# Performance work log

Measured on AMD Instinct MI355X. Metric: run time of the kernel, lower is better.

## Reference

```python
import jax, jax.numpy as jnp
import numpy as np

B, L, F = 16, 2048, 512


def setup_inputs() -> dict:
    key = jax.random.key(0)
    k1, k2 = jax.random.split(key)
    feature = jax.random.normal(k1, (B, L, F), dtype=jnp.float32)
    noise = jax.random.normal(k2, (B, L, L), dtype=jnp.float32)
    return {"feature": feature, "noise": noise}


def reference(feature, noise):
    # augmenting_path = softmax over last dim of (B, L, L) gaussian noise
    augmenting_path = jax.nn.softmax(noise, axis=-1)
    # einsum 'bij,bjf->bif': mix frames along the sequence dim
    augmented_feature = jnp.einsum('bij,bjf->bif', augmenting_path, feature)
    return augmented_feature
```

## Files before the change

kernel.cpp:

```cpp
#include <hip/hip_runtime.h>
#include <hip/hip_bf16.h>


#define NB 16
#define SL 2048
#define NF 512
#define TM 64
#define BK 32
#define NT 512

typedef __bf16 bf16x8 __attribute__((ext_vector_type(8)));
typedef float  f32x4  __attribute__((ext_vector_type(4)));

__device__ __forceinline__ unsigned short f2bf(float x) {
    union { float f; unsigned int u; } v; v.f = x;
    return (unsigned short)((v.u + 0x7FFFu + ((v.u >> 16) & 1u)) >> 16);
}

__global__ __launch_bounds__(256, 4)
void feat_panelize(const float* __restrict__ feat, unsigned short* __restrict__ featP) {
    __shared__ unsigned short Lt[32][270];
    const int t  = threadIdx.x;
    const int n0 = blockIdx.x * 256;
    const int kb = blockIdx.y;
    const int b  = blockIdx.z;
    const float* src = feat + ((size_t)b * SL + (size_t)kb * BK) * NF + n0;
    const int j  = t >> 3;
    const int c0 = (t & 7) << 2;
    #pragma unroll
    for (int c = 0; c < 8; ++c) {
        const float4 v = *(const float4*)(src + (size_t)j * NF + c0 + (c << 5));
        unsigned short* p = &Lt[j][c0 + (c << 5)];
        p[0] = f2bf(v.x); p[1] = f2bf(v.y); p[2] = f2bf(v.z); p[3] = f2bf(v.w);
    }
    __syncthreads();
    unsigned int w[16];
    #pragma unroll
    for (int m = 0; m < 16; ++m)
        w[m] = (unsigned int)Lt[2 * m][t] | ((unsigned int)Lt[2 * m + 1][t] << 16);
    unsigned short* dst = featP + ((size_t)(b * 64 + kb) * NF + (size_t)(n0 + t)) * BK;
    #pragma unroll
    for (int c = 0; c < 4; ++c)
        *(uint4*)(dst + (c << 3)) = *(const uint4*)&w[c << 2];
}

__global__ __launch_bounds__(NT, 2)
void frame_augment(const float* __restrict__ noise,
                   const unsigned short* __restrict__ featP,
                   float* __restrict__ out) {
    __shared__ __align__(16) unsigned short As[TM][40];
    __shared__ __align__(16) unsigned short Bs[NF][40];
    __shared__ float part[TM][9];
    __shared__ float linv[TM];

    const int tid  = threadIdx.x;
    const int lane = tid & 63;
    const int wv   = tid >> 6;
    const int b    = blockIdx.y;
    const int i0   = blockIdx.x * TM;

    const float* noise_b = noise + ((size_t)b * SL + i0) * SL;
    float*       out_b   = out   + ((size_t)b * SL + i0) * NF;

    const int a_row = tid >> 3;
    const int a_col = (tid & 7) << 2;
    const int fm = lane & 15;
    const int fq = lane >> 4;

    f32x4 acc[4][4];
    #pragma unroll
    for (int mi = 0; mi < 4; ++mi)
        #pragma unroll
        for (int ni = 0; ni < 4; ++ni)
            acc[mi][ni] = (f32x4){0.f, 0.f, 0.f, 0.f};

    float rowsum = 0.f;
    const float* a_src = noise_b + (size_t)a_row * SL + a_col;

    for (int kb = 0; kb < SL / BK; ++kb) {
        const float4 nv = *(const float4*)(a_src + kb * BK);
        const float e0 = __expf(nv.x), e1 = __expf(nv.y);
        const float e2 = __expf(nv.z), e3 = __expf(nv.w);
        rowsum += (e0 + e1) + (e2 + e3);
        uint2 ap;
        ap.x = (unsigned int)f2bf(e0) | ((unsigned int)f2bf(e1) << 16);
        ap.y = (unsigned int)f2bf(e2) | ((unsigned int)f2bf(e3) << 16);
        *(uint2*)&As[a_row][a_col] = ap;

        const unsigned short* panel = featP + (size_t)(b * 64 + kb) * NF * BK;
        #pragma unroll
        for (int c = 0; c < 4; ++c) {
            const int q = tid + (c << 9);
            const uint4 d = *(const uint4*)(panel + (size_t)q * 8);
            *(uint4*)&Bs[q >> 2][(q & 3) << 3] = d;
        }
        __syncthreads();

        bf16x8 af[4], bfr[4];
        #pragma unroll
        for (int mi = 0; mi < 4; ++mi)
            af[mi] = *(const bf16x8*)&As[mi * 16 + fm][fq << 3];
        #pragma unroll
        for (int ni = 0; ni < 4; ++ni)
            bfr[ni] = *(const bf16x8*)&Bs[(wv << 6) + ni * 16 + fm][fq << 3];
        #pragma unroll
        for (int mi = 0; mi < 4; ++mi)
            #pragma unroll
            for (int ni = 0; ni < 4; ++ni)
                acc[mi][ni] = __builtin_amdgcn_mfma_f32_16x16x32_bf16(
                    af[mi], bfr[ni], acc[mi][ni], 0, 0, 0);
        __syncthreads();
    }

    part[a_row][tid & 7] = rowsum;
    __syncthreads();
    if (tid < TM) {
        float s = 0.f;
        #pragma unroll
        for (int q = 0; q < 8; ++q) s += part[tid][q];
        linv[tid] = 1.0f / s;
    }
    __syncthreads();

    #pragma unroll
    for (int mi = 0; mi < 4; ++mi) {
        #pragma unroll
        for (int r = 0; r < 4; ++r) {
            const int row = mi * 16 + (fq << 2) + r;
            const float sc = linv[row];
            float* orow = out_b + (size_t)row * NF + (wv << 6) + fm;
            #pragma unroll
            for (int ni = 0; ni < 4; ++ni)
                orow[ni * 16] = acc[mi][ni][r] * sc;
        }
    }
}

extern "C" void kernel_launch(void* const* d_in, const int* in_sizes, int n_in,
                              void* d_out, int out_size, void* d_ws, size_t ws_size,
                              hipStream_t stream) {
    (void)in_sizes; (void)n_in; (void)out_size; (void)ws_size;
    const float* feat  = (const float*)d_in[0];
    const float* noise = (const float*)d_in[1];
    float* outp = (float*)d_out;
    unsigned short* featP = (unsigned short*)d_ws;

    feat_panelize<<<dim3(NF / 256, SL / BK, NB), 256, 0, stream>>>(feat, featP);
    frame_augment<<<dim3(SL / TM, NB), NT, 0, stream>>>(noise, featP, outp);
}
```

Measured before the change: 469.0 us.

## Double-buffer LDS with direct global-to-LDS loads, double M tile, remap blocks

The main GEMM kernel now uses double-buffered LDS tiles. The feature panel for the next K step is loaded straight into LDS with global_load_lds, and the noise for two steps ahead is prefetched into registers, so loads overlap the MFMA work. The row tile grows from 64 to 128, which halves how often each block re-reads the feature panels, and the grid is flattened with a batch-interleaved block order to improve L2 locality. The LDS rows lose their padding, which may cause bank conflicts. The larger accumulator also raises register pressure and could reduce occupancy.

```diff
diff --git a/kernel.cpp b/kernel.cpp
--- a/kernel.cpp
+++ b/kernel.cpp
@@ -5,16 +5,17 @@
 #define NB 16
 #define SL 2048
 #define NF 512
-#define TM 64
+#define TM 128
 #define BK 32
 #define NT 512
+#define NKB (SL / BK)
 
 typedef __bf16 bf16x8 __attribute__((ext_vector_type(8)));
 typedef float  f32x4  __attribute__((ext_vector_type(4)));
 
-__device__ __forceinline__ unsigned short f2bf(float x) {
+__device__ __forceinline__ unsigned int f2bf(float x) {
     union { float f; unsigned int u; } v; v.f = x;
-    return (unsigned short)((v.u + 0x7FFFu + ((v.u >> 16) & 1u)) >> 16);
+    return (v.u + 0x7FFFu + ((v.u >> 16) & 1u)) >> 16;
 }
 
 __global__ __launch_bounds__(256, 4)
@@ -31,14 +32,15 @@
     for (int c = 0; c < 8; ++c) {
         const float4 v = *(const float4*)(src + (size_t)j * NF + c0 + (c << 5));
         unsigned short* p = &Lt[j][c0 + (c << 5)];
-        p[0] = f2bf(v.x); p[1] = f2bf(v.y); p[2] = f2bf(v.z); p[3] = f2bf(v.w);
+        p[0] = (unsigned short)f2bf(v.x); p[1] = (unsigned short)f2bf(v.y);
+        p[2] = (unsigned short)f2bf(v.z); p[3] = (unsigned short)f2bf(v.w);
     }
     __syncthreads();
     unsigned int w[16];
     #pragma unroll
     for (int m = 0; m < 16; ++m)
         w[m] = (unsigned int)Lt[2 * m][t] | ((unsigned int)Lt[2 * m + 1][t] << 16);
-    unsigned short* dst = featP + ((size_t)(b * 64 + kb) * NF + (size_t)(n0 + t)) * BK;
+    unsigned short* dst = featP + ((size_t)(b * NKB + kb) * NF + (size_t)(n0 + t)) * BK;
     #pragma unroll
     for (int c = 0; c < 4; ++c)
         *(uint4*)(dst + (c << 3)) = *(const uint4*)&w[c << 2];
@@ -48,63 +50,98 @@
 void frame_augment(const float* __restrict__ noise,
                    const unsigned short* __restrict__ featP,
                    float* __restrict__ out) {
-    __shared__ __align__(16) unsigned short As[TM][40];
-    __shared__ __align__(16) unsigned short Bs[NF][40];
-    __shared__ float part[TM][9];
+    __shared__ __align__(16) unsigned short As[2][TM][BK];
+    __shared__ __align__(16) unsigned short Bs[2][NF][BK];
+    __shared__ float part[TM][4];
     __shared__ float linv[TM];
 
     const int tid  = threadIdx.x;
     const int lane = tid & 63;
     const int wv   = tid >> 6;
-    const int b    = blockIdx.y;
-    const int i0   = blockIdx.x * TM;
+    const int n    = blockIdx.x;
+    const int b    = ((n & 7) << 1) | ((n >> 3) & 1);
+    const int i0   = (n >> 4) * TM;
 
     const float* noise_b = noise + ((size_t)b * SL + i0) * SL;
-    float*       out_b   = out   + ((size_t)b * SL + i0) * NF;
+    const unsigned short* featB = featP + (size_t)b * NKB * NF * BK;
+    float* out_b = out + ((size_t)b * SL + i0) * NF;
 
-    const int a_row = tid >> 3;
-    const int a_col = (tid & 7) << 2;
+    const int ar = tid >> 2;
+    const int ac = (tid & 3) << 3;
     const int fm = lane & 15;
     const int fq = lane >> 4;
 
-    f32x4 acc[4][4];
+    f32x4 acc[8][4];
     #pragma unroll
-    for (int mi = 0; mi < 4; ++mi)
+    for (int mi = 0; mi < 8; ++mi)
         #pragma unroll
         for (int ni = 0; ni < 4; ++ni)
             acc[mi][ni] = (f32x4){0.f, 0.f, 0.f, 0.f};
 
     float rowsum = 0.f;
-    const float* a_src = noise_b + (size_t)a_row * SL + a_col;
+    const float* a_src = noise_b + (size_t)ar * SL + ac;
 
-    for (int kb = 0; kb < SL / BK; ++kb) {
-        const float4 nv = *(const float4*)(a_src + kb * BK);
-        const float e0 = __expf(nv.x), e1 = __expf(nv.y);
-        const float e2 = __expf(nv.z), e3 = __expf(nv.w);
-        rowsum += (e0 + e1) + (e2 + e3);
-        uint2 ap;
-        ap.x = (unsigned int)f2bf(e0) | ((unsigned int)f2bf(e1) << 16);
-        ap.y = (unsigned int)f2bf(e2) | ((unsigned int)f2bf(e3) << 16);
-        *(uint2*)&As[a_row][a_col] = ap;
-
-        const unsigned short* panel = featP + (size_t)(b * 64 + kb) * NF * BK;
+    float4 nv0 = *(const float4*)(a_src);
+    float4 nv1 = *(const float4*)(a_src + 4);
+    {
+        const float e0=__expf(nv0.x), e1=__expf(nv0.y), e2=__expf(nv0.z), e3=__expf(nv0.w);
+        const float e4=__expf(nv1.x), e5=__expf(nv1.y), e6=__expf(nv1.z), e7=__expf(nv1.w);
+        rowsum += ((e0+e1)+(e2+e3)) + ((e4+e5)+(e6+e7));
+        uint4 p;
+        p.x = f2bf(e0) | (f2bf(e1) << 16);  p.y = f2bf(e2) | (f2bf(e3) << 16);
+        p.z = f2bf(e4) | (f2bf(e5) << 16);  p.w = f2bf(e6) | (f2bf(e7) << 16);
+        *(uint4*)&As[0][ar][ac] = p;
+    }
+    {
+        const unsigned short* panel = featB;
         #pragma unroll
         for (int c = 0; c < 4; ++c) {
-            const int q = tid + (c << 9);
-            const uint4 d = *(const uint4*)(panel + (size_t)q * 8);
-            *(uint4*)&Bs[q >> 2][(q & 3) << 3] = d;
+            const int q = (c << 9) + tid;
+            __builtin_amdgcn_global_load_lds(
+                (const __attribute__((address_space(1))) unsigned int*)(panel + (size_t)q * 8),
+                (__attribute__((address_space(3))) unsigned int*)&Bs[0][q >> 2][(q & 3) << 3],
+                16, 0, 0);
         }
-        __syncthreads();
+    }
+    nv0 = *(const float4*)(a_src + BK);
+    nv1 = *(const float4*)(a_src + BK + 4);
+    __syncthreads();
 
-        bf16x8 af[4], bfr[4];
+    for (int kb = 0; kb < NKB; ++kb) {
+        const int cur = kb & 1, nxt = cur ^ 1;
+
+        if (kb + 1 < NKB) {
+            const unsigned short* panel = featB + (size_t)(kb + 1) * NF * BK;
+            #pragma unroll
+            for (int c = 0; c < 4; ++c) {
+                const int q = (c << 9) + tid;
+                __builtin_amdgcn_global_load_lds(
+                    (const __attribute__((address_space(1))) unsigned int*)(panel + (size_t)q * 8),
+                    (__attribute__((address_space(3))) unsigned int*)&Bs[nxt][q >> 2][(q & 3) << 3],
+                    16, 0, 0);
+            }
+            const float e0=__expf(nv0.x), e1=__expf(nv0.y), e2=__expf(nv0.z), e3=__expf(nv0.w);
+            const float e4=__expf(nv1.x), e5=__expf(nv1.y), e6=__expf(nv1.z), e7=__expf(nv1.w);
+            rowsum += ((e0+e1)+(e2+e3)) + ((e4+e5)+(e6+e7));
+            uint4 p;
+            p.x = f2bf(e0) | (f2bf(e1) << 16);  p.y = f2bf(e2) | (f2bf(e3) << 16);
+            p.z = f2bf(e4) | (f2bf(e5) << 16);  p.w = f2bf(e6) | (f2bf(e7) << 16);
+            *(uint4*)&As[nxt][ar][ac] = p;
+        }
+        if (kb + 2 < NKB) {
+            nv0 = *(const float4*)(a_src + (size_t)(kb + 2) * BK);
+            nv1 = *(const float4*)(a_src + (size_t)(kb + 2) * BK + 4);
+        }
+
+        bf16x8 af[8], bfr[4];
         #pragma unroll
-        for (int mi = 0; mi < 4; ++mi)
-            af[mi] = *(const bf16x8*)&As[mi * 16 + fm][fq << 3];
+        for (int mi = 0; mi < 8; ++mi)
+            af[mi] = *(const bf16x8*)&As[cur][mi * 16 + fm][fq << 3];
         #pragma unroll
         for (int ni = 0; ni < 4; ++ni)
-            bfr[ni] = *(const bf16x8*)&Bs[(wv << 6) + ni * 16 + fm][fq << 3];
+            bfr[ni] = *(const bf16x8*)&Bs[cur][(wv << 6) + ni * 16 + fm][fq << 3];
         #pragma unroll
-        for (int mi = 0; mi < 4; ++mi)
+        for (int mi = 0; mi < 8; ++mi)
             #pragma unroll
             for (int ni = 0; ni < 4; ++ni)
                 acc[mi][ni] = __builtin_amdgcn_mfma_f32_16x16x32_bf16(
@@ -112,18 +149,16 @@
         __syncthreads();
     }
 
-    part[a_row][tid & 7] = rowsum;
+    part[ar][tid & 3] = rowsum;
     __syncthreads();
     if (tid < TM) {
-        float s = 0.f;
-        #pragma unroll
-        for (int q = 0; q < 8; ++q) s += part[tid][q];
-        linv[tid] = 1.0f / s;
+        const float* q = part[tid];
+        linv[tid] = 1.0f / (((q[0] + q[1]) + (q[2] + q[3])));
     }
     __syncthreads();
 
     #pragma unroll
-    for (int mi = 0; mi < 4; ++mi) {
+    for (int mi = 0; mi < 8; ++mi) {
         #pragma unroll
         for (int r = 0; r < 4; ++r) {
             const int row = mi * 16 + (fq << 2) + r;
@@ -145,6 +180,6 @@
     float* outp = (float*)d_out;
     unsigned short* featP = (unsigned short*)d_ws;
 
-    feat_panelize<<<dim3(NF / 256, SL / BK, NB), 256, 0, stream>>>(feat, featP);
-    frame_augment<<<dim3(SL / TM, NB), NT, 0, stream>>>(noise, featP, outp);
+    feat_panelize<<<dim3(NF / 256, NKB, NB), 256, 0, stream>>>(feat, featP);
+    frame_augment<<<dim3(SL / TM * NB), NT, 0, stream>>>(noise, featP, outp);
 }
```

After: 461.3 us. Within noise of the previous version (-1.6%).
